# Kernel tuning notes

Measured on AMD Instinct MI355X. Metric: run time of the kernel, lower is better.

The kernel has to match this reference:

```python
import jax, jax.numpy as jnp
import numpy as np

H = 2048      # hidden_size
NH = 16       # num_attention_heads
HD = H // NH  # head_dim = 128
B, S = 2, 2048
ROPE_BASE = 10000.0


def setup_inputs() -> dict:
    key = jax.random.key(0)
    ks = jax.random.split(key, 9)
    init = 0.02
    inp = {
        "hidden_states": jax.random.normal(ks[0], (B, S, H), dtype=jnp.float32),
        # torch nn.Linear weights are [out_features, in_features]
        "wq": jax.random.normal(ks[1], (H, H), dtype=jnp.float32) * init,
        "bq": jnp.zeros((H,), dtype=jnp.float32),
        "wk": jax.random.normal(ks[2], (H, H), dtype=jnp.float32) * init,
        "bk": jnp.zeros((H,), dtype=jnp.float32),
        "wv": jax.random.normal(ks[3], (H, H), dtype=jnp.float32) * init,
        "bv": jnp.zeros((H,), dtype=jnp.float32),
        "wo": jax.random.normal(ks[4], (H, H), dtype=jnp.float32) * init,
        "bo": jnp.zeros((H,), dtype=jnp.float32),
    }
    return inp


def _rope_cos_sin(seq_len, dim, dtype):
    # standard RoPE tables: [seq_len, dim]
    inv_freq = 1.0 / (ROPE_BASE ** (jnp.arange(0, dim, 2, dtype=jnp.float32) / dim))
    freqs = jnp.arange(seq_len, dtype=jnp.float32)[:, None] * inv_freq[None, :]
    emb = jnp.concatenate([freqs, freqs], axis=-1)  # [S, dim]
    return jnp.cos(emb).astype(dtype), jnp.sin(emb).astype(dtype)


def _rotate_half(x):
    half = x.shape[-1] // 2
    return jnp.concatenate([-x[..., half:], x[..., :half]], axis=-1)


def reference(hidden_states, wq, bq, wk, bk, wv, bv, wo, bo):
    b, s, h = hidden_states.shape
    scale = HD ** -0.5

    def proj(x, w, bias):
        y = jnp.einsum("bsh,oh->bso", x, w) + bias
        # -> [b, nh, s, hd]
        return y.reshape(b, s, NH, HD).transpose(0, 2, 1, 3)

    q = proj(hidden_states, wq, bq)
    k = proj(hidden_states, wk, bk)
    v = proj(hidden_states, wv, bv)

    # rotary embeddings on q, k
    cos, sin = _rope_cos_sin(s, HD, q.dtype)  # [s, hd]
    q = q * cos + _rotate_half(q) * sin
    k = k * cos + _rotate_half(k) * sin

    # causal additive mask [s, s]
    mask = jnp.triu(jnp.full((s, s), -1e9, dtype=q.dtype), k=1)

    scores = jnp.einsum("bhqd,bhkd->bhqk", q, k) * scale + mask
    probs = jax.nn.softmax(scores, axis=-1)
    attn = jnp.einsum("bhqk,bhkd->bhqd", probs, v)
    attn = attn.transpose(0, 2, 1, 3).reshape(b, s, h)
    out = jnp.einsum("bsh,oh->bso", attn, wo) + bo
    return out
```

## Files before the change

### kernel.cpp

```cpp
#include <hip/hip_runtime.h>

typedef unsigned short u16;
typedef __attribute__((ext_vector_type(8))) __bf16 bf16x8;
typedef __attribute__((ext_vector_type(4))) float f32x4;
typedef __attribute__((ext_vector_type(4))) u16 u16x4;
typedef __attribute__((ext_vector_type(8))) u16 u16x8;

constexpr int S = 2048;
constexpr int H = 2048;
constexpr int NH = 16;
constexpr int HD = 128;
constexpr int M = 4096;
constexpr float SCALE = 0.08838834764831845f;

__device__ __forceinline__ u16 f2bf(float f) {
  union { float f; unsigned u; } v; v.f = f;
  unsigned r = v.u + 0x7fffu + ((v.u >> 16) & 1u);
  return (u16)(r >> 16);
}
__device__ __forceinline__ float bf2f(u16 u) {
  union { unsigned u; float f; } v; v.u = ((unsigned)u) << 16;
  return v.f;
}
__device__ __forceinline__ unsigned cvt_pk_bf16(float lo, float hi) {
  unsigned r;
  asm("v_cvt_pk_bf16_f32 %0, %1, %2" : "=v"(r) : "v"(lo), "v"(hi));
  return r;
}

__device__ __forceinline__ void gld16(const u16* g, u16* l) {
  __builtin_amdgcn_global_load_lds(
      (const __attribute__((address_space(1))) void*)g,
      (__attribute__((address_space(3))) void*)l, 16, 0, 0);
}

__global__ __launch_bounds__(256) void cast_kernel(const float* __restrict__ in,
                                                   u16* __restrict__ out, int n) {
  int i = (blockIdx.x * 256 + threadIdx.x) * 4;
  if (i >= n) return;
  float4 v = *(const float4*)(in + i);
  u16x4 o;
  o[0] = f2bf(v.x); o[1] = f2bf(v.y); o[2] = f2bf(v.z); o[3] = f2bf(v.w);
  *(u16x4*)(out + i) = o;
}

__global__ __launch_bounds__(256) void cast4_kernel(const float* __restrict__ i0,
                                                    const float* __restrict__ i1,
                                                    const float* __restrict__ i2,
                                                    const float* __restrict__ i3,
                                                    u16* o0, u16* o1, u16* o2, u16* o3) {
  const float* in; u16* out;
  switch (blockIdx.y) {
    case 0: in = i0; out = o0; break;
    case 1: in = i1; out = o1; break;
    case 2: in = i2; out = o2; break;
    default: in = i3; out = o3; break;
  }
  int i = (blockIdx.x * 256 + threadIdx.x) * 4;
  float4 v = *(const float4*)(in + i);
  u16x4 o;
  o[0] = f2bf(v.x); o[1] = f2bf(v.y); o[2] = f2bf(v.z); o[3] = f2bf(v.w);
  *(u16x4*)(out + i) = o;
}

__global__ __launch_bounds__(256) void rope_table_k(float* __restrict__ tab) {
  int i = blockIdx.x * 256 + threadIdx.x;
  if (i >= S * 64) return;
  int s = i >> 6, d = i & 63;
  float freq = expf(-(float)d * (9.210340371976184f / 64.f));
  float ang = (float)s * freq;
  tab[i * 2]     = cosf(ang);
  tab[i * 2 + 1] = sinf(ang);
}

__global__ __launch_bounds__(256) void rope_apply2_k(u16* __restrict__ Qb, u16* __restrict__ Kb,
                                                     const float* __restrict__ tab) {
  u16* X = blockIdx.y ? Kb : Qb;
  const float sc = blockIdx.y ? 1.f : SCALE;
  int i = blockIdx.x * 256 + threadIdx.x;
  int j0 = (i & 7) * 8;
  int h  = (i >> 3) & 15;
  int m  = i >> 7;
  int s  = m & (S - 1);
  u16* p = X + (size_t)m * H + h * HD;
  u16x8 lo = *(u16x8*)(p + j0);
  u16x8 hi = *(u16x8*)(p + 64 + j0);
  u16x8 nlo, nhi;
  const float* tb = tab + ((size_t)s * 64 + j0) * 2;
  #pragma unroll
  for (int j = 0; j < 8; ++j) {
    float c = tb[j * 2], sn = tb[j * 2 + 1];
    float xl = bf2f(lo[j]), xh = bf2f(hi[j]);
    nlo[j] = f2bf((xl * c - xh * sn) * sc);
    nhi[j] = f2bf((xh * c + xl * sn) * sc);
  }
  *(u16x8*)(p + j0) = nlo;
  *(u16x8*)(p + 64 + j0) = nhi;
}


__global__ __launch_bounds__(256) void gemm_qkv(const u16* __restrict__ A,
                                                const u16* __restrict__ Wq,
                                                const u16* __restrict__ Wk,
                                                const u16* __restrict__ Wv,
                                                const float* __restrict__ bq,
                                                const float* __restrict__ bk,
                                                const float* __restrict__ bv,
                                                u16* __restrict__ Qb,
                                                u16* __restrict__ Kb,
                                                u16* __restrict__ Vt) {
  __shared__ u16 As[128 * 32];
  __shared__ u16 Bs[128 * 32];
  const int z = blockIdx.z;
  const u16* Bw = (z == 0) ? Wq : (z == 1) ? Wk : Wv;
  const float* bias = (z == 0) ? bq : (z == 1) ? bk : bv;
  const int t = threadIdx.x;
  const int w = t >> 6, l = t & 63;
  const int wr = w >> 1, wc = w & 1;
  const int lr = l & 15, lg = l >> 4;
  const int brow = blockIdx.y * 128, bcol = blockIdx.x * 128;

  f32x4 acc[4][4] = {};

  const int srow = t >> 2;
  const int scol = (t & 3) * 8;
  const u16* ga = A  + (size_t)(brow + srow) * H + scol;
  const u16* gb = Bw + (size_t)(bcol + srow) * H + scol;
  u16* la = As + srow * 32 + scol;
  u16* lb = Bs + srow * 32 + scol;

  for (int kt = 0; kt < H; kt += 32) {
    gld16(ga + kt,          la);
    gld16(ga + kt + 64 * H, la + 64 * 32);
    gld16(gb + kt,          lb);
    gld16(gb + kt + 64 * H, lb + 64 * 32);
    __syncthreads();
    bf16x8 af[4], bf[4];
    #pragma unroll
    for (int m = 0; m < 4; ++m)
      af[m] = *(const bf16x8*)(As + (wr * 64 + m * 16 + lr) * 32 + lg * 8);
    #pragma unroll
    for (int n = 0; n < 4; ++n)
      bf[n] = *(const bf16x8*)(Bs + (wc * 64 + n * 16 + lr) * 32 + lg * 8);
    #pragma unroll
    for (int m = 0; m < 4; ++m)
      #pragma unroll
      for (int n = 0; n < 4; ++n)
        acc[m][n] = __builtin_amdgcn_mfma_f32_16x16x32_bf16(af[m], bf[n], acc[m][n], 0, 0, 0);
    __syncthreads();
  }

  #pragma unroll
  for (int m = 0; m < 4; ++m) {
    const int row0 = brow + wr * 64 + m * 16 + lg * 4;
    #pragma unroll
    for (int n = 0; n < 4; ++n) {
      const int col = bcol + wc * 64 + n * 16 + lr;
      const float bv2 = bias[col];
      if (z < 2) {
        u16* C = z ? Kb : Qb;
        #pragma unroll
        for (int r = 0; r < 4; ++r)
          C[(size_t)(row0 + r) * H + col] = f2bf(acc[m][n][r] + bv2);
      } else {
        const int hh = col >> 7, d = col & 127;
        const int b = row0 >> 11, s0 = row0 & (S - 1);
        u16x4 pk;
        #pragma unroll
        for (int r = 0; r < 4; ++r) pk[r] = f2bf(acc[m][n][r] + bv2);
        *(u16x4*)(Vt + ((size_t)((b * 16 + hh) * 128 + d)) * S + s0) = pk;
      }
    }
  }
}

__global__ __launch_bounds__(256) void gemm_out(const u16* __restrict__ A,
                                                const u16* __restrict__ Bw,
                                                const float* __restrict__ bias,
                                                float* __restrict__ Cout) {
  __shared__ u16 As[128 * 32];
  __shared__ u16 Bs[128 * 32];
  const int t = threadIdx.x;
  const int w = t >> 6, l = t & 63;
  const int wr = w >> 1, wc = w & 1;
  const int lr = l & 15, lg = l >> 4;
  const int brow = blockIdx.y * 128, bcol = blockIdx.x * 128;

  f32x4 acc[4][4] = {};

  const int srow = t >> 2;
  const int scol = (t & 3) * 8;
  const u16* ga = A  + (size_t)(brow + srow) * H + scol;
  const u16* gb = Bw + (size_t)(bcol + srow) * H + scol;
  u16* la = As + srow * 32 + scol;
  u16* lb = Bs + srow * 32 + scol;

  for (int kt = 0; kt < H; kt += 32) {
    gld16(ga + kt,          la);
    gld16(ga + kt + 64 * H, la + 64 * 32);
    gld16(gb + kt,          lb);
    gld16(gb + kt + 64 * H, lb + 64 * 32);
    __syncthreads();
    bf16x8 af[4], bf[4];
    #pragma unroll
    for (int m = 0; m < 4; ++m)
      af[m] = *(const bf16x8*)(As + (wr * 64 + m * 16 + lr) * 32 + lg * 8);
    #pragma unroll
    for (int n = 0; n < 4; ++n)
      bf[n] = *(const bf16x8*)(Bs + (wc * 64 + n * 16 + lr) * 32 + lg * 8);
    #pragma unroll
    for (int m = 0; m < 4; ++m)
      #pragma unroll
      for (int n = 0; n < 4; ++n)
        acc[m][n] = __builtin_amdgcn_mfma_f32_16x16x32_bf16(af[m], bf[n], acc[m][n], 0, 0, 0);
    __syncthreads();
  }

  #pragma unroll
  for (int m = 0; m < 4; ++m) {
    const int row0 = brow + wr * 64 + m * 16 + lg * 4;
    #pragma unroll
    for (int n = 0; n < 4; ++n) {
      const int col = bcol + wc * 64 + n * 16 + lr;
      const float bv2 = bias[col];
      #pragma unroll
      for (int r = 0; r < 4; ++r)
        Cout[(size_t)(row0 + r) * H + col] = acc[m][n][r] + bv2;
    }
  }
}

__global__ __launch_bounds__(256) void attn_fwd(const u16* __restrict__ Q,
                                                const u16* __restrict__ Kx,
                                                const u16* __restrict__ Vt,
                                                u16* __restrict__ O) {
  const int id = blockIdx.x;
  const int xcd = id & 7, slot = id >> 3;
  const int bh = (slot >> 4) * 8 + xcd;
  const int pid = slot & 15;
  const int b = bh >> 4, h = bh & 15;
  const int t = threadIdx.x, w = t >> 6, l = t & 63;
  const int lr = l & 15, lg = l >> 4;
  const int swz = lr & 7;

  __shared__ u16 Ks[2][64 * 128];
  __shared__ u16 Vs[2][128 * 64];
  __shared__ u16 P_lds[4][16 * 64];
  u16* pw = &P_lds[w][0];

  const u16* kbase = Kx + (size_t)(b * S) * H + h * HD;
  const u16* vbase = Vt + (size_t)bh * HD * S;

  auto stageK = [&](int bf, int k0) {
    #pragma unroll
    for (int it = 0; it < 4; ++it) {
      int c = it * 256 + t;
      int row = c >> 4, j = c & 15;
      gld16(kbase + (size_t)(k0 + row) * H + ((j ^ (row & 7)) * 8), &Ks[bf][0] + c * 8);
    }
  };
  auto stageV = [&](int bf, int k0) {
    #pragma unroll
    for (int it = 0; it < 4; ++it) {
      int c = it * 256 + t;
      int row = c >> 3, j = c & 7;
      gld16(vbase + (size_t)row * S + k0 + ((j ^ (row & 7)) * 8), &Vs[bf][0] + c * 8);
    }
  };

  int cur = 0;
  for (int qi = 0; qi < 2; ++qi) {
    const int qt = qi ? pid : (31 - pid);
    const int q0 = qt * 64 + w * 16;

    bf16x8 qa[4];
    const u16* qbase = Q + (size_t)(b * S + q0 + lr) * H + h * HD;
    #pragma unroll
    for (int ks = 0; ks < 4; ++ks)
      qa[ks] = *(const bf16x8*)(qbase + ks * 32 + lg * 8);

    f32x4 acc[8] = {};
    float mrun[4], lrun[4];
    #pragma unroll
    for (int r = 0; r < 4; ++r) { mrun[r] = -1e30f; lrun[r] = 0.f; }

    __syncthreads();
    stageK(cur, 0);
    stageV(cur, 0);
    __syncthreads();

    for (int kt = 0; kt <= qt; ++kt) {
      if (kt < qt) {
        stageK(cur ^ 1, (kt + 1) * 64);
        stageV(cur ^ 1, (kt + 1) * 64);
      }
      const u16* kl = &Ks[cur][0];
      const u16* vl = &Vs[cur][0];

      f32x4 sc[4] = {};
      __builtin_amdgcn_s_setprio(1);
      #pragma unroll
      for (int ks = 0; ks < 4; ++ks) {
        #pragma unroll
        for (int f = 0; f < 4; ++f) {
          bf16x8 kf = *(const bf16x8*)(kl + (f * 16 + lr) * 128 + (((ks * 4 + lg) ^ swz) * 8));
          sc[f] = __builtin_amdgcn_mfma_f32_16x16x32_bf16(qa[ks], kf, sc[f], 0, 0, 0);
        }
      }
      __builtin_amdgcn_s_setprio(0);
      const bool diag = (kt == qt);
      float p[4][4];
      #pragma unroll
      for (int f = 0; f < 4; ++f)
        #pragma unroll
        for (int r = 0; r < 4; ++r) {
          float v = sc[f][r];
          if (diag && (f * 16 + lr > w * 16 + lg * 4 + r)) v = -1e30f;
          p[f][r] = v;
        }
      float mx[4];
      #pragma unroll
      for (int r = 0; r < 4; ++r) {
        float m0 = fmaxf(fmaxf(p[0][r], p[1][r]), fmaxf(p[2][r], p[3][r]));
        m0 = fmaxf(m0, __shfl_xor(m0, 1));
        m0 = fmaxf(m0, __shfl_xor(m0, 2));
        m0 = fmaxf(m0, __shfl_xor(m0, 4));
        m0 = fmaxf(m0, __shfl_xor(m0, 8));
        mx[r] = m0;
      }
      bool grow = (mx[0] > mrun[0] + 8.f) || (mx[1] > mrun[1] + 8.f) ||
                  (mx[2] > mrun[2] + 8.f) || (mx[3] > mrun[3] + 8.f);
      if (__any(grow)) {
        float resc[4];
        #pragma unroll
        for (int r = 0; r < 4; ++r) {
          float mnew = fmaxf(mrun[r], mx[r]);
          resc[r] = __expf(mrun[r] - mnew);
          mrun[r] = mnew;
          lrun[r] *= resc[r];
        }
        #pragma unroll
        for (int fd = 0; fd < 8; ++fd) {
          f32x4 a = acc[fd];
          a[0] *= resc[0]; a[1] *= resc[1]; a[2] *= resc[2]; a[3] *= resc[3];
          acc[fd] = a;
        }
      }
      #pragma unroll
      for (int r = 0; r < 4; ++r) {
        float sum = 0.f;
        #pragma unroll
        for (int f = 0; f < 4; ++f) {
          float e = __expf(p[f][r] - mrun[r]);
          p[f][r] = e;
          sum += e;
        }
        sum += __shfl_xor(sum, 1);
        sum += __shfl_xor(sum, 2);
        sum += __shfl_xor(sum, 4);
        sum += __shfl_xor(sum, 8);
        lrun[r] += sum;
      }
      {
        const int r0 = lg * 4;
        #pragma unroll
        for (int f = 0; f < 4; ++f) {
          const int col = f * 16 + lr;
          unsigned w01 = cvt_pk_bf16(p[f][0], p[f][1]);
          unsigned w23 = cvt_pk_bf16(p[f][2], p[f][3]);
          pw[(r0 + 0) * 64 + (col ^ (((r0 + 0) & 7) << 3))] = (u16)(w01 & 0xffffu);
          pw[(r0 + 1) * 64 + (col ^ (((r0 + 1) & 7) << 3))] = (u16)(w01 >> 16);
          pw[(r0 + 2) * 64 + (col ^ (((r0 + 2) & 7) << 3))] = (u16)(w23 & 0xffffu);
          pw[(r0 + 3) * 64 + (col ^ (((r0 + 3) & 7) << 3))] = (u16)(w23 >> 16);
        }
      }
      __builtin_amdgcn_s_setprio(1);
      #pragma unroll
      for (int ks = 0; ks < 2; ++ks) {
        int col0 = ks * 32 + lg * 8;
        bf16x8 pa = *(const bf16x8*)(pw + lr * 64 + (col0 ^ (swz << 3)));
        #pragma unroll
        for (int fd = 0; fd < 8; ++fd) {
          bf16x8 vb = *(const bf16x8*)(vl + (fd * 16 + lr) * 64 + (((ks * 4 + lg) ^ swz) * 8));
          acc[fd] = __builtin_amdgcn_mfma_f32_16x16x32_bf16(pa, vb, acc[fd], 0, 0, 0);
        }
      }
      __builtin_amdgcn_s_setprio(0);
      __syncthreads();
      cur ^= 1;
    }

    u16* ob = O + (size_t)(b * S + q0 + lg * 4) * H + h * HD;
    #pragma unroll
    for (int r = 0; r < 4; ++r) {
      float inv = 1.f / lrun[r];
      #pragma unroll
      for (int fd = 0; fd < 8; ++fd)
        ob[(size_t)r * H + fd * 16 + lr] = f2bf(acc[fd][r] * inv);
    }
  }
}

extern "C" void kernel_launch(void* const* d_in, const int* in_sizes, int n_in,
                              void* d_out, int out_size, void* d_ws, size_t ws_size,
                              hipStream_t stream) {
  const float* x  = (const float*)d_in[0];
  const float* wq = (const float*)d_in[1];
  const float* bq = (const float*)d_in[2];
  const float* wk = (const float*)d_in[3];
  const float* bk = (const float*)d_in[4];
  const float* wv = (const float*)d_in[5];
  const float* bv = (const float*)d_in[6];
  const float* wo = (const float*)d_in[7];
  const float* bo = (const float*)d_in[8];

  char* ws = (char*)d_ws;
  u16*   xb  = (u16*)(ws);
  u16*   wqb = (u16*)(ws + (16ull << 20));
  u16*   wkb = (u16*)(ws + (24ull << 20));
  u16*   wvb = (u16*)(ws + (32ull << 20));
  u16*   wob = (u16*)(ws + (40ull << 20));
  u16*   Qb  = (u16*)(ws + (48ull << 20));
  u16*   Kb  = (u16*)(ws + (64ull << 20));
  u16*   Vt  = (u16*)(ws + (80ull << 20));
  u16*   Ob  = (u16*)(ws + (96ull << 20));
  float* tab = (float*)(ws + (112ull << 20));

  cast_kernel<<<M * H / 1024, 256, 0, stream>>>(x, xb, M * H);
  cast4_kernel<<<dim3(H * H / 1024, 4), 256, 0, stream>>>(wq, wk, wv, wo, wqb, wkb, wvb, wob);
  rope_table_k<<<(S * 64 + 255) / 256, 256, 0, stream>>>(tab);

  gemm_qkv<<<dim3(H / 128, M / 128, 3), 256, 0, stream>>>(xb, wqb, wkb, wvb, bq, bk, bv, Qb, Kb, Vt);

  rope_apply2_k<<<dim3(M * NH * 8 / 256, 2), 256, 0, stream>>>(Qb, Kb, tab);

  attn_fwd<<<dim3(512), 256, 0, stream>>>(Qb, Kb, Vt, Ob);

  gemm_out<<<dim3(H / 128, M / 128), 256, 0, stream>>>(Ob, wob, bo, (float*)d_out);
}
```

Baseline: 314.9 us.

## Replace QKV and output GEMMs with 256x256 8-wave pipelined GEMM

Both projection GEMMs are replaced by a shared 256x256-tile kernel that uses 512 threads, a BK=64 double-buffered LDS pipeline, XOR-swizzled LDS layout and explicit waitcnt/barrier scheduling. Blocks are remapped across XCDs. The larger tiles raise arithmetic intensity, and the interleaved global-to-LDS staging is meant to hide memory latency behind MFMA work. The costs are heavy register pressure (32 accumulators per lane) and 128 KB of LDS per block. The output GEMM also launches only 128 blocks, which may underfill the GPU.

Result: slower. 328.3 us (+4.3%).

```diff
diff --git a/kernel.cpp b/kernel.cpp
--- a/kernel.cpp
+++ b/kernel.cpp
@@ -27,12 +27,19 @@
   asm("v_cvt_pk_bf16_f32 %0, %1, %2" : "=v"(r) : "v"(lo), "v"(hi));
   return r;
 }
+__device__ __forceinline__ f32x4 MFMA16(bf16x8 a, bf16x8 b, f32x4 c) {
+  return __builtin_amdgcn_mfma_f32_16x16x32_bf16(a, b, c, 0, 0, 0);
+}
 
 __device__ __forceinline__ void gld16(const u16* g, u16* l) {
   __builtin_amdgcn_global_load_lds(
       (const __attribute__((address_space(1))) void*)g,
       (__attribute__((address_space(3))) void*)l, 16, 0, 0);
 }
+
+#define SBAR  { __builtin_amdgcn_sched_barrier(0); __builtin_amdgcn_s_barrier(); __builtin_amdgcn_sched_barrier(0); }
+#define LGKM0 { asm volatile("s_waitcnt lgkmcnt(0)" ::: "memory"); __builtin_amdgcn_sched_barrier(0); }
+#define VM(N) { asm volatile("s_waitcnt vmcnt(" #N ")" ::: "memory"); }
 
 __global__ __launch_bounds__(256) void cast_kernel(const float* __restrict__ in,
                                                    u16* __restrict__ out, int n) {
@@ -98,136 +105,173 @@
   *(u16x8*)(p + 64 + j0) = nhi;
 }
 
-
-__global__ __launch_bounds__(256) void gemm_qkv(const u16* __restrict__ A,
-                                                const u16* __restrict__ Wq,
-                                                const u16* __restrict__ Wk,
-                                                const u16* __restrict__ Wv,
-                                                const float* __restrict__ bq,
-                                                const float* __restrict__ bk,
-                                                const float* __restrict__ bv,
-                                                u16* __restrict__ Qb,
-                                                u16* __restrict__ Kb,
-                                                u16* __restrict__ Vt) {
-  __shared__ u16 As[128 * 32];
-  __shared__ u16 Bs[128 * 32];
-  const int z = blockIdx.z;
-  const u16* Bw = (z == 0) ? Wq : (z == 1) ? Wk : Wv;
-  const float* bias = (z == 0) ? bq : (z == 1) ? bk : bv;
+__device__ __forceinline__ void gemm8_body(const u16* __restrict__ srcA,
+                                           const u16* __restrict__ srcB,
+                                           const float* __restrict__ bias,
+                                           void* __restrict__ Cout,
+                                           int emode, int brow, int bcol,
+                                           u16* AsL, u16* BsL) {
   const int t = threadIdx.x;
   const int w = t >> 6, l = t & 63;
-  const int wr = w >> 1, wc = w & 1;
+  const int wr = w >> 2, wc = w & 3;
   const int lr = l & 15, lg = l >> 4;
-  const int brow = blockIdx.y * 128, bcol = blockIdx.x * 128;
-
-  f32x4 acc[4][4] = {};
-
-  const int srow = t >> 2;
-  const int scol = (t & 3) * 8;
-  const u16* ga = A  + (size_t)(brow + srow) * H + scol;
-  const u16* gb = Bw + (size_t)(bcol + srow) * H + scol;
-  u16* la = As + srow * 32 + scol;
-  u16* lb = Bs + srow * 32 + scol;
-
-  for (int kt = 0; kt < H; kt += 32) {
-    gld16(ga + kt,          la);
-    gld16(ga + kt + 64 * H, la + 64 * 32);
-    gld16(gb + kt,          lb);
-    gld16(gb + kt + 64 * H, lb + 64 * 32);
-    __syncthreads();
-    bf16x8 af[4], bf[4];
-    #pragma unroll
-    for (int m = 0; m < 4; ++m)
-      af[m] = *(const bf16x8*)(As + (wr * 64 + m * 16 + lr) * 32 + lg * 8);
-    #pragma unroll
-    for (int n = 0; n < 4; ++n)
-      bf[n] = *(const bf16x8*)(Bs + (wc * 64 + n * 16 + lr) * 32 + lg * 8);
-    #pragma unroll
-    for (int m = 0; m < 4; ++m)
-      #pragma unroll
-      for (int n = 0; n < 4; ++n)
-        acc[m][n] = __builtin_amdgcn_mfma_f32_16x16x32_bf16(af[m], bf[n], acc[m][n], 0, 0, 0);
-    __syncthreads();
+  const int swz = lr & 7;
+
+  f32x4 acc[8][4] = {};
+  bf16x8 af[4][2], bA[2][2], bB[2][2];
+
+  const int c0r = t >> 3,        c0j = t & 7;
+  const int c1r = 64 + (t >> 3), c1j = t & 7;
+
+  #define STAGE(SRC, DSTB, BUF, HALF, TILE) do {                                   \
+    u16* _d = (DSTB) + (BUF) * (256 * 64) + (HALF) * (128 * 64);                   \
+    const u16* _s = (SRC) + ((size_t)((HALF) * 128)) * H + (TILE) * 64;            \
+    gld16(_s + (size_t)c0r * H + ((c0j ^ (c0r & 7)) * 8), _d + t * 8);             \
+    gld16(_s + (size_t)c1r * H + ((c1j ^ (c1r & 7)) * 8), _d + (512 + t) * 8);     \
+  } while (0)
+
+  #define LDA4(BUF, MB) do {                                                       \
+    const u16* _b = AsL + (BUF) * (256 * 64) + (wr * 128 + lr) * 64;               \
+    _Pragma("unroll") for (int i = 0; i < 4; ++i) {                                \
+      af[i][0] = *(const bf16x8*)(_b + ((MB) + i) * (16 * 64) + ((lg ^ swz) * 8)); \
+      af[i][1] = *(const bf16x8*)(_b + ((MB) + i) * (16 * 64) + (((4 + lg) ^ swz) * 8)); \
+    } } while (0)
+
+  #define LDB2(BUF, BF, NB) do {                                                   \
+    const u16* _b = BsL + (BUF) * (256 * 64) + (wc * 64 + lr) * 64;                \
+    _Pragma("unroll") for (int i = 0; i < 2; ++i) {                                \
+      BF[i][0] = *(const bf16x8*)(_b + ((NB) + i) * (16 * 64) + ((lg ^ swz) * 8)); \
+      BF[i][1] = *(const bf16x8*)(_b + ((NB) + i) * (16 * 64) + (((4 + lg) ^ swz) * 8)); \
+    } } while (0)
+
+  #define MM16(MB, BF, NB) do {                                                    \
+    __builtin_amdgcn_s_setprio(1);                                                 \
+    _Pragma("unroll") for (int i = 0; i < 4; ++i)                                  \
+      _Pragma("unroll") for (int n = 0; n < 2; ++n) {                              \
+        acc[(MB) + i][(NB) + n] = MFMA16(af[i][0], BF[n][0], acc[(MB) + i][(NB) + n]); \
+        acc[(MB) + i][(NB) + n] = MFMA16(af[i][1], BF[n][1], acc[(MB) + i][(NB) + n]); \
+      }                                                                            \
+    __builtin_amdgcn_s_setprio(0);                                                 \
+  } while (0)
+
+  STAGE(srcB, BsL, 0, 0, 0); STAGE(srcB, BsL, 0, 1, 0);
+  STAGE(srcA, AsL, 0, 0, 0); STAGE(srcA, AsL, 0, 1, 0);
+  STAGE(srcB, BsL, 1, 0, 1);
+  VM(2);
+  SBAR;
+
+  for (int J = 0; J < 16; ++J) {
+    const int u = 2 * J;
+    const bool more = (J < 15);
+    LDA4(0, 0); LDB2(0, bA, 0);
+    STAGE(srcB, BsL, 1, 1, u + 1);
+    SBAR; LGKM0;
+    MM16(0, bA, 0);
+    SBAR;
+    LDA4(0, 4);
+    STAGE(srcA, AsL, 1, 0, u + 1);
+    SBAR; LGKM0;
+    MM16(4, bA, 0);
+    SBAR;
+    LDB2(0, bB, 2);
+    STAGE(srcA, AsL, 1, 1, u + 1);
+    SBAR; LGKM0;
+    MM16(4, bB, 2);
+    SBAR;
+    LDA4(0, 0);
+    if (more) STAGE(srcB, BsL, 0, 0, u + 2);
+    SBAR; LGKM0;
+    MM16(0, bB, 2);
+    if (more) { VM(2); } else { VM(0); }
+    SBAR;
+    LDA4(1, 0); LDB2(1, bA, 0);
+    if (more) STAGE(srcB, BsL, 0, 1, u + 2);
+    SBAR; LGKM0;
+    MM16(0, bA, 0);
+    SBAR;
+    LDA4(1, 4);
+    if (more) STAGE(srcA, AsL, 0, 0, u + 2);
+    SBAR; LGKM0;
+    MM16(4, bA, 0);
+    SBAR;
+    LDB2(1, bB, 2);
+    if (more) STAGE(srcA, AsL, 0, 1, u + 2);
+    SBAR; LGKM0;
+    MM16(4, bB, 2);
+    SBAR;
+    LDA4(1, 0);
+    if (more) STAGE(srcB, BsL, 1, 0, u + 3);
+    SBAR; LGKM0;
+    MM16(0, bB, 2);
+    if (more) VM(2);
+    SBAR;
   }
 
   #pragma unroll
-  for (int m = 0; m < 4; ++m) {
-    const int row0 = brow + wr * 64 + m * 16 + lg * 4;
+  for (int m = 0; m < 8; ++m) {
+    const int row0 = brow + wr * 128 + m * 16 + lg * 4;
     #pragma unroll
     for (int n = 0; n < 4; ++n) {
       const int col = bcol + wc * 64 + n * 16 + lr;
-      const float bv2 = bias[col];
-      if (z < 2) {
-        u16* C = z ? Kb : Qb;
+      const float bv = bias[col];
+      if (emode == 0) {
+        float* C = (float*)Cout;
         #pragma unroll
         for (int r = 0; r < 4; ++r)
-          C[(size_t)(row0 + r) * H + col] = f2bf(acc[m][n][r] + bv2);
+          C[(size_t)(row0 + r) * H + col] = acc[m][n][r] + bv;
+      } else if (emode == 1) {
+        u16* C = (u16*)Cout;
+        #pragma unroll
+        for (int r = 0; r < 4; ++r)
+          C[(size_t)(row0 + r) * H + col] = f2bf(acc[m][n][r] + bv);
       } else {
         const int hh = col >> 7, d = col & 127;
         const int b = row0 >> 11, s0 = row0 & (S - 1);
         u16x4 pk;
         #pragma unroll
-        for (int r = 0; r < 4; ++r) pk[r] = f2bf(acc[m][n][r] + bv2);
-        *(u16x4*)(Vt + ((size_t)((b * 16 + hh) * 128 + d)) * S + s0) = pk;
+        for (int r = 0; r < 4; ++r) pk[r] = f2bf(acc[m][n][r] + bv);
+        *(u16x4*)((u16*)Cout + ((size_t)((b * 16 + hh) * 128 + d)) * S + s0) = pk;
       }
     }
   }
-}
-
-__global__ __launch_bounds__(256) void gemm_out(const u16* __restrict__ A,
-                                                const u16* __restrict__ Bw,
-                                                const float* __restrict__ bias,
-                                                float* __restrict__ Cout) {
-  __shared__ u16 As[128 * 32];
-  __shared__ u16 Bs[128 * 32];
-  const int t = threadIdx.x;
-  const int w = t >> 6, l = t & 63;
-  const int wr = w >> 1, wc = w & 1;
-  const int lr = l & 15, lg = l >> 4;
-  const int brow = blockIdx.y * 128, bcol = blockIdx.x * 128;
-
-  f32x4 acc[4][4] = {};
-
-  const int srow = t >> 2;
-  const int scol = (t & 3) * 8;
-  const u16* ga = A  + (size_t)(brow + srow) * H + scol;
-  const u16* gb = Bw + (size_t)(bcol + srow) * H + scol;
-  u16* la = As + srow * 32 + scol;
-  u16* lb = Bs + srow * 32 + scol;
-
-  for (int kt = 0; kt < H; kt += 32) {
-    gld16(ga + kt,          la);
-    gld16(ga + kt + 64 * H, la + 64 * 32);
-    gld16(gb + kt,          lb);
-    gld16(gb + kt + 64 * H, lb + 64 * 32);
-    __syncthreads();
-    bf16x8 af[4], bf[4];
-    #pragma unroll
-    for (int m = 0; m < 4; ++m)
-      af[m] = *(const bf16x8*)(As + (wr * 64 + m * 16 + lr) * 32 + lg * 8);
-    #pragma unroll
-    for (int n = 0; n < 4; ++n)
-      bf[n] = *(const bf16x8*)(Bs + (wc * 64 + n * 16 + lr) * 32 + lg * 8);
-    #pragma unroll
-    for (int m = 0; m < 4; ++m)
-      #pragma unroll
-      for (int n = 0; n < 4; ++n)
-        acc[m][n] = __builtin_amdgcn_mfma_f32_16x16x32_bf16(af[m], bf[n], acc[m][n], 0, 0, 0);
-    __syncthreads();
-  }
-
-  #pragma unroll
-  for (int m = 0; m < 4; ++m) {
-    const int row0 = brow + wr * 64 + m * 16 + lg * 4;
-    #pragma unroll
-    for (int n = 0; n < 4; ++n) {
-      const int col = bcol + wc * 64 + n * 16 + lr;
-      const float bv2 = bias[col];
-      #pragma unroll
-      for (int r = 0; r < 4; ++r)
-        Cout[(size_t)(row0 + r) * H + col] = acc[m][n][r] + bv2;
-    }
-  }
+  #undef STAGE
+  #undef LDA4
+  #undef LDB2
+  #undef MM16
+}
+
+__global__ __launch_bounds__(512, 2) void gemm8_qkv(const u16* __restrict__ xb,
+                                                    const u16* __restrict__ wqb,
+                                                    const u16* __restrict__ wkb,
+                                                    const u16* __restrict__ wvb,
+                                                    const float* __restrict__ bq,
+                                                    const float* __restrict__ bk,
+                                                    const float* __restrict__ bv,
+                                                    u16* Qb, u16* Kb, u16* Vt) {
+  __shared__ u16 AsL[2 * 256 * 64];
+  __shared__ u16 BsL[2 * 256 * 64];
+  const int id = blockIdx.x;
+  const int lin = (id & 7) * 48 + (id >> 3);
+  const int bz = lin >> 7, rem = lin & 127;
+  const int bx = rem & 7, by = rem >> 3;
+  const u16* Bw = (bz == 0) ? wqb : (bz == 1) ? wkb : wvb;
+  const float* bias = (bz == 0) ? bq : (bz == 1) ? bk : bv;
+  void* out = (bz == 0) ? (void*)Qb : (bz == 1) ? (void*)Kb : (void*)Vt;
+  gemm8_body(xb + (size_t)(by * 256) * H, Bw + (size_t)(bx * 256) * H,
+             bias, out, (bz == 2) ? 2 : 1, by * 256, bx * 256, AsL, BsL);
+}
+
+__global__ __launch_bounds__(512, 2) void gemm8_out(const u16* __restrict__ A,
+                                                    const u16* __restrict__ W,
+                                                    const float* __restrict__ bias,
+                                                    float* __restrict__ C) {
+  __shared__ u16 AsL[2 * 256 * 64];
+  __shared__ u16 BsL[2 * 256 * 64];
+  const int id = blockIdx.x;
+  const int lin = (id & 7) * 16 + (id >> 3);
+  const int bx = lin & 7, by = lin >> 3;
+  gemm8_body(A + (size_t)(by * 256) * H, W + (size_t)(bx * 256) * H,
+             bias, (void*)C, 0, by * 256, bx * 256, AsL, BsL);
 }
 
 __global__ __launch_bounds__(256) void attn_fwd(const u16* __restrict__ Q,
@@ -430,11 +474,11 @@
   cast4_kernel<<<dim3(H * H / 1024, 4), 256, 0, stream>>>(wq, wk, wv, wo, wqb, wkb, wvb, wob);
   rope_table_k<<<(S * 64 + 255) / 256, 256, 0, stream>>>(tab);
 
-  gemm_qkv<<<dim3(H / 128, M / 128, 3), 256, 0, stream>>>(xb, wqb, wkb, wvb, bq, bk, bv, Qb, Kb, Vt);
+  gemm8_qkv<<<384, 512, 0, stream>>>(xb, wqb, wkb, wvb, bq, bk, bv, Qb, Kb, Vt);
 
   rope_apply2_k<<<dim3(M * NH * 8 / 256, 2), 256, 0, stream>>>(Qb, Kb, tab);
 
-  attn_fwd<<<dim3(512), 256, 0, stream>>>(Qb, Kb, Vt, Ob);
-
-  gemm_out<<<dim3(H / 128, M / 128), 256, 0, stream>>>(Ob, wob, bo, (float*)d_out);
-}
+  attn_fwd<<<512, 256, 0, stream>>>(Qb, Kb, Vt, Ob);
+
+  gemm8_out<<<128, 512, 0, stream>>>(Ob, wob, bo, (float*)d_out);
+}
```

## Rewrite projection GEMMs as 8-wave double-buffered pipelined kernels with fused QKV weight

Applied to the files above, without the earlier changes.

Replaces the simple 128x128 single-buffered QKV and output GEMMs with a shared templated body using 512 threads, 256-row tiles, K=64 double-buffered LDS with XOR swizzle, explicit waitcnt/barrier scheduling and MFMA priority. The Q, K and V weights are cast into one concatenated matrix and the biases concatenated, so a single GEMM with 192-wide column tiles covers all three projections. Block IDs are remapped per XCD for L2 locality. The aim is better MFMA utilisation and load/compute overlap, at the cost of fragile hand-tuned vmcnt gating and higher register and LDS pressure.

Result: faster. 275.5 us (-12.5%).

```diff
diff --git a/kernel.cpp b/kernel.cpp
--- a/kernel.cpp
+++ b/kernel.cpp
@@ -27,12 +27,18 @@
   asm("v_cvt_pk_bf16_f32 %0, %1, %2" : "=v"(r) : "v"(lo), "v"(hi));
   return r;
 }
+__device__ __forceinline__ f32x4 MFMA16(bf16x8 a, bf16x8 b, f32x4 c) {
+  return __builtin_amdgcn_mfma_f32_16x16x32_bf16(a, b, c, 0, 0, 0);
+}
 
 __device__ __forceinline__ void gld16(const u16* g, u16* l) {
   __builtin_amdgcn_global_load_lds(
       (const __attribute__((address_space(1))) void*)g,
       (__attribute__((address_space(3))) void*)l, 16, 0, 0);
 }
+
+#define SBAR  { __builtin_amdgcn_sched_barrier(0); __builtin_amdgcn_s_barrier(); __builtin_amdgcn_sched_barrier(0); }
+#define LGKM0 { asm volatile("s_waitcnt lgkmcnt(0)" ::: "memory"); __builtin_amdgcn_sched_barrier(0); }
 
 __global__ __launch_bounds__(256) void cast_kernel(const float* __restrict__ in,
                                                    u16* __restrict__ out, int n) {
@@ -61,6 +67,15 @@
   u16x4 o;
   o[0] = f2bf(v.x); o[1] = f2bf(v.y); o[2] = f2bf(v.z); o[3] = f2bf(v.w);
   *(u16x4*)(out + i) = o;
+}
+
+__global__ __launch_bounds__(256) void concat_bias_k(const float* __restrict__ bq,
+                                                     const float* __restrict__ bk,
+                                                     const float* __restrict__ bv,
+                                                     float* __restrict__ bqkv) {
+  int i = blockIdx.x * 256 + threadIdx.x;
+  const float* src = (i < 2048) ? bq : (i < 4096) ? bk : bv;
+  bqkv[i] = src[i & 2047];
 }
 
 __global__ __launch_bounds__(256) void rope_table_k(float* __restrict__ tab) {
@@ -98,136 +113,156 @@
   *(u16x8*)(p + 64 + j0) = nhi;
 }
 
-
-__global__ __launch_bounds__(256) void gemm_qkv(const u16* __restrict__ A,
-                                                const u16* __restrict__ Wq,
-                                                const u16* __restrict__ Wk,
-                                                const u16* __restrict__ Wv,
-                                                const float* __restrict__ bq,
-                                                const float* __restrict__ bk,
-                                                const float* __restrict__ bv,
-                                                u16* __restrict__ Qb,
-                                                u16* __restrict__ Kb,
-                                                u16* __restrict__ Vt) {
-  __shared__ u16 As[128 * 32];
-  __shared__ u16 Bs[128 * 32];
-  const int z = blockIdx.z;
-  const u16* Bw = (z == 0) ? Wq : (z == 1) ? Wk : Wv;
-  const float* bias = (z == 0) ? bq : (z == 1) ? bk : bv;
+template<int NW, int EMODE>
+__device__ __forceinline__ void gemm_body(const u16* __restrict__ A,
+                                          const u16* __restrict__ Bw,
+                                          const float* __restrict__ bias,
+                                          void* __restrict__ out0, void* __restrict__ out1,
+                                          void* __restrict__ out2,
+                                          int brow, int bcol,
+                                          u16* AsL, u16* BsL) {
   const int t = threadIdx.x;
   const int w = t >> 6, l = t & 63;
-  const int wr = w >> 1, wc = w & 1;
+  const int wr = w >> 2, wc = w & 3;
   const int lr = l & 15, lg = l >> 4;
-  const int brow = blockIdx.y * 128, bcol = blockIdx.x * 128;
-
-  f32x4 acc[4][4] = {};
-
-  const int srow = t >> 2;
-  const int scol = (t & 3) * 8;
-  const u16* ga = A  + (size_t)(brow + srow) * H + scol;
-  const u16* gb = Bw + (size_t)(bcol + srow) * H + scol;
-  u16* la = As + srow * 32 + scol;
-  u16* lb = Bs + srow * 32 + scol;
-
-  for (int kt = 0; kt < H; kt += 32) {
-    gld16(ga + kt,          la);
-    gld16(ga + kt + 64 * H, la + 64 * 32);
-    gld16(gb + kt,          lb);
-    gld16(gb + kt + 64 * H, lb + 64 * 32);
-    __syncthreads();
-    bf16x8 af[4], bf[4];
-    #pragma unroll
-    for (int m = 0; m < 4; ++m)
-      af[m] = *(const bf16x8*)(As + (wr * 64 + m * 16 + lr) * 32 + lg * 8);
-    #pragma unroll
-    for (int n = 0; n < 4; ++n)
-      bf[n] = *(const bf16x8*)(Bs + (wc * 64 + n * 16 + lr) * 32 + lg * 8);
-    #pragma unroll
-    for (int m = 0; m < 4; ++m)
-      #pragma unroll
-      for (int n = 0; n < 4; ++n)
-        acc[m][n] = __builtin_amdgcn_mfma_f32_16x16x32_bf16(af[m], bf[n], acc[m][n], 0, 0, 0);
-    __syncthreads();
+  const int swz = lr & 7;
+
+  f32x4 acc[8][NW] = {};
+  bf16x8 af[4], b0[NW], b1[NW];
+
+  const int sr = t >> 3, sj = t & 7;
+
+  auto STAGE_A = [&](int BUF, int HALF, int TILE) {
+    u16* d = AsL + BUF * (256 * 64) + HALF * (128 * 64);
+    const u16* sp = A + (size_t)(brow + HALF * 128) * H + TILE * 64;
+    gld16(sp + (size_t)sr * H        + ((sj ^ (sr & 7)) * 8), d + t * 8);
+    gld16(sp + (size_t)(64 + sr) * H + ((sj ^ (sr & 7)) * 8), d + (512 + t) * 8);
+  };
+  auto STAGE_B = [&](int BUF, int TILE) {
+    u16* d = BsL + BUF * (NW * 64 * 64);
+    const u16* sp = Bw + (size_t)bcol * H + TILE * 64;
+    #pragma unroll
+    for (int i = 0; i < NW; ++i)
+      gld16(sp + (size_t)(i * 64 + sr) * H + ((sj ^ (sr & 7)) * 8),
+            d + (i * 512 + t) * 8);
+  };
+  auto LDA = [&](int BUF, int KH, int MB) {
+    const u16* base = AsL + BUF * (256 * 64) + (wr * 128 + MB * 16 + lr) * 64;
+    #pragma unroll
+    for (int i = 0; i < 4; ++i)
+      af[i] = *(const bf16x8*)(base + i * (16 * 64) + (((KH * 4 + lg) ^ swz) * 8));
+  };
+  auto LDB = [&](int BUF, int KH, bf16x8* bb) {
+    const u16* base = BsL + BUF * (NW * 64 * 64) + (wc * (NW * 16) + lr) * 64;
+    #pragma unroll
+    for (int n = 0; n < NW; ++n)
+      bb[n] = *(const bf16x8*)(base + n * (16 * 64) + (((KH * 4 + lg) ^ swz) * 8));
+  };
+  auto MM = [&](int MB, bf16x8* bb) {
+    __builtin_amdgcn_s_setprio(1);
+    #pragma unroll
+    for (int i = 0; i < 4; ++i)
+      #pragma unroll
+      for (int n = 0; n < NW; ++n)
+        acc[MB + i][n] = MFMA16(af[i], bb[n], acc[MB + i][n]);
+    __builtin_amdgcn_s_setprio(0);
+  };
+  auto GATE = [&]() {
+    if constexpr (NW == 3) { asm volatile("s_waitcnt vmcnt(3)" ::: "memory"); }
+    else                   { asm volatile("s_waitcnt vmcnt(2)" ::: "memory"); }
+  };
+
+  STAGE_A(0, 0, 0); STAGE_A(0, 1, 0);
+  STAGE_B(0, 0);
+  STAGE_B(1, 1);
+  GATE();
+  SBAR;
+
+  for (int J = 0; J < 16; ++J) {
+    const int u = 2 * J;
+    const bool more = (J < 15);
+    LDA(0, 0, 0); LDB(0, 0, b0);
+    STAGE_A(1, 0, u + 1);
+    SBAR; LGKM0; MM(0, b0); SBAR;
+    LDA(0, 0, 4);
+    STAGE_A(1, 1, u + 1);
+    SBAR; LGKM0; MM(4, b0); SBAR;
+    LDA(0, 1, 0); LDB(0, 1, b1);
+    SBAR; LGKM0; MM(0, b1); SBAR;
+    LDA(0, 1, 4);
+    if (more) STAGE_B(0, u + 2);
+    SBAR; LGKM0; MM(4, b1);
+    if (more) { GATE(); } else { asm volatile("s_waitcnt vmcnt(0)" ::: "memory"); }
+    SBAR;
+    LDA(1, 0, 0); LDB(1, 0, b0);
+    if (more) STAGE_A(0, 0, u + 2);
+    SBAR; LGKM0; MM(0, b0); SBAR;
+    LDA(1, 0, 4);
+    if (more) STAGE_A(0, 1, u + 2);
+    SBAR; LGKM0; MM(4, b0); SBAR;
+    LDA(1, 1, 0); LDB(1, 1, b1);
+    SBAR; LGKM0; MM(0, b1); SBAR;
+    LDA(1, 1, 4);
+    if (more) STAGE_B(1, u + 3);
+    SBAR; LGKM0; MM(4, b1);
+    if (more) { GATE(); SBAR; }
   }
 
   #pragma unroll
-  for (int m = 0; m < 4; ++m) {
-    const int row0 = brow + wr * 64 + m * 16 + lg * 4;
-    #pragma unroll
-    for (int n = 0; n < 4; ++n) {
-      const int col = bcol + wc * 64 + n * 16 + lr;
-      const float bv2 = bias[col];
-      if (z < 2) {
-        u16* C = z ? Kb : Qb;
+  for (int m = 0; m < 8; ++m) {
+    const int row0 = brow + wr * 128 + m * 16 + lg * 4;
+    #pragma unroll
+    for (int n = 0; n < NW; ++n) {
+      const int gcol0 = bcol + wc * (NW * 16) + n * 16;
+      const float bv = bias[gcol0 + lr];
+      if constexpr (EMODE == 0) {
+        float* C = (float*)out0;
         #pragma unroll
         for (int r = 0; r < 4; ++r)
-          C[(size_t)(row0 + r) * H + col] = f2bf(acc[m][n][r] + bv2);
+          C[(size_t)(row0 + r) * H + gcol0 + lr] = acc[m][n][r] + bv;
       } else {
-        const int hh = col >> 7, d = col & 127;
-        const int b = row0 >> 11, s0 = row0 & (S - 1);
-        u16x4 pk;
-        #pragma unroll
-        for (int r = 0; r < 4; ++r) pk[r] = f2bf(acc[m][n][r] + bv2);
-        *(u16x4*)(Vt + ((size_t)((b * 16 + hh) * 128 + d)) * S + s0) = pk;
+        const int sel = gcol0 >> 11;
+        const int col = (gcol0 & 2047) + lr;
+        if (sel < 2) {
+          u16* C = sel ? (u16*)out1 : (u16*)out0;
+          #pragma unroll
+          for (int r = 0; r < 4; ++r)
+            C[(size_t)(row0 + r) * H + col] = f2bf(acc[m][n][r] + bv);
+        } else {
+          const int hh = col >> 7, d = col & 127;
+          const int b = row0 >> 11, s0 = row0 & (S - 1);
+          u16x4 pk;
+          #pragma unroll
+          for (int r = 0; r < 4; ++r) pk[r] = f2bf(acc[m][n][r] + bv);
+          *(u16x4*)((u16*)out2 + ((size_t)((b * 16 + hh) * 128 + d)) * S + s0) = pk;
+        }
       }
     }
   }
 }
 
-__global__ __launch_bounds__(256) void gemm_out(const u16* __restrict__ A,
-                                                const u16* __restrict__ Bw,
-                                                const float* __restrict__ bias,
-                                                float* __restrict__ Cout) {
-  __shared__ u16 As[128 * 32];
-  __shared__ u16 Bs[128 * 32];
-  const int t = threadIdx.x;
-  const int w = t >> 6, l = t & 63;
-  const int wr = w >> 1, wc = w & 1;
-  const int lr = l & 15, lg = l >> 4;
-  const int brow = blockIdx.y * 128, bcol = blockIdx.x * 128;
-
-  f32x4 acc[4][4] = {};
-
-  const int srow = t >> 2;
-  const int scol = (t & 3) * 8;
-  const u16* ga = A  + (size_t)(brow + srow) * H + scol;
-  const u16* gb = Bw + (size_t)(bcol + srow) * H + scol;
-  u16* la = As + srow * 32 + scol;
-  u16* lb = Bs + srow * 32 + scol;
-
-  for (int kt = 0; kt < H; kt += 32) {
-    gld16(ga + kt,          la);
-    gld16(ga + kt + 64 * H, la + 64 * 32);
-    gld16(gb + kt,          lb);
-    gld16(gb + kt + 64 * H, lb + 64 * 32);
-    __syncthreads();
-    bf16x8 af[4], bf[4];
-    #pragma unroll
-    for (int m = 0; m < 4; ++m)
-      af[m] = *(const bf16x8*)(As + (wr * 64 + m * 16 + lr) * 32 + lg * 8);
-    #pragma unroll
-    for (int n = 0; n < 4; ++n)
-      bf[n] = *(const bf16x8*)(Bs + (wc * 64 + n * 16 + lr) * 32 + lg * 8);
-    #pragma unroll
-    for (int m = 0; m < 4; ++m)
-      #pragma unroll
-      for (int n = 0; n < 4; ++n)
-        acc[m][n] = __builtin_amdgcn_mfma_f32_16x16x32_bf16(af[m], bf[n], acc[m][n], 0, 0, 0);
-    __syncthreads();
-  }
-
-  #pragma unroll
-  for (int m = 0; m < 4; ++m) {
-    const int row0 = brow + wr * 64 + m * 16 + lg * 4;
-    #pragma unroll
-    for (int n = 0; n < 4; ++n) {
-      const int col = bcol + wc * 64 + n * 16 + lr;
-      const float bv2 = bias[col];
-      #pragma unroll
-      for (int r = 0; r < 4; ++r)
-        Cout[(size_t)(row0 + r) * H + col] = acc[m][n][r] + bv2;
-    }
-  }
+__global__ __launch_bounds__(512, 2) void gemm_qkv8(const u16* __restrict__ xb,
+                                                    const u16* __restrict__ wqkv,
+                                                    const float* __restrict__ bqkv,
+                                                    u16* Qb, u16* Kb, u16* Vt) {
+  __shared__ u16 AsL[2 * 256 * 64];
+  __shared__ u16 BsL[2 * 192 * 64];
+  const int id = blockIdx.x;
+  const int xcd = id & 7, sid = id >> 3;
+  const int bx = xcd * 4 + (sid & 3), by = sid >> 2;
+  gemm_body<3, 3>(xb, wqkv, bqkv, Qb, Kb, Vt, by * 256, bx * 192, AsL, BsL);
+}
+
+__global__ __launch_bounds__(512, 2) void gemm_o8(const u16* __restrict__ A,
+                                                  const u16* __restrict__ W,
+                                                  const float* __restrict__ bias,
+                                                  float* __restrict__ C) {
+  __shared__ u16 AsL[2 * 256 * 64];
+  __shared__ u16 BsL[2 * 128 * 64];
+  const int id = blockIdx.x;
+  const int xcd = id & 7, sid = id >> 3;
+  const int bx = xcd * 2 + (sid & 1), by = sid >> 1;
+  gemm_body<2, 0>(A, W, bias, C, nullptr, nullptr, by * 256, bx * 128, AsL, BsL);
 }
 
 __global__ __launch_bounds__(256) void attn_fwd(const u16* __restrict__ Q,
@@ -415,26 +450,27 @@
   const float* bo = (const float*)d_in[8];
 
   char* ws = (char*)d_ws;
-  u16*   xb  = (u16*)(ws);
-  u16*   wqb = (u16*)(ws + (16ull << 20));
-  u16*   wkb = (u16*)(ws + (24ull << 20));
-  u16*   wvb = (u16*)(ws + (32ull << 20));
-  u16*   wob = (u16*)(ws + (40ull << 20));
-  u16*   Qb  = (u16*)(ws + (48ull << 20));
-  u16*   Kb  = (u16*)(ws + (64ull << 20));
-  u16*   Vt  = (u16*)(ws + (80ull << 20));
-  u16*   Ob  = (u16*)(ws + (96ull << 20));
-  float* tab = (float*)(ws + (112ull << 20));
+  u16*   xb    = (u16*)(ws);
+  u16*   wqkvb = (u16*)(ws + (16ull << 20));
+  u16*   wob   = (u16*)(ws + (40ull << 20));
+  u16*   Qb    = (u16*)(ws + (48ull << 20));
+  u16*   Kb    = (u16*)(ws + (64ull << 20));
+  u16*   Vt    = (u16*)(ws + (80ull << 20));
+  u16*   Ob    = (u16*)(ws + (96ull << 20));
+  float* tab   = (float*)(ws + (112ull << 20));
+  float* bqkv  = (float*)(ws + (113ull << 20));
 
   cast_kernel<<<M * H / 1024, 256, 0, stream>>>(x, xb, M * H);
-  cast4_kernel<<<dim3(H * H / 1024, 4), 256, 0, stream>>>(wq, wk, wv, wo, wqb, wkb, wvb, wob);
+  cast4_kernel<<<dim3(H * H / 1024, 4), 256, 0, stream>>>(
+      wq, wk, wv, wo, wqkvb, wqkvb + (size_t)H * H, wqkvb + 2ull * H * H, wob);
   rope_table_k<<<(S * 64 + 255) / 256, 256, 0, stream>>>(tab);
-
-  gemm_qkv<<<dim3(H / 128, M / 128, 3), 256, 0, stream>>>(xb, wqb, wkb, wvb, bq, bk, bv, Qb, Kb, Vt);
+  concat_bias_k<<<24, 256, 0, stream>>>(bq, bk, bv, bqkv);
+
+  gemm_qkv8<<<512, 512, 0, stream>>>(xb, wqkvb, bqkv, Qb, Kb, Vt);
 
   rope_apply2_k<<<dim3(M * NH * 8 / 256, 2), 256, 0, stream>>>(Qb, Kb, tab);
 
-  attn_fwd<<<dim3(512), 256, 0, stream>>>(Qb, Kb, Vt, Ob);
-
-  gemm_out<<<dim3(H / 128, M / 128), 256, 0, stream>>>(Ob, wob, bo, (float*)d_out);
-}
+  attn_fwd<<<512, 256, 0, stream>>>(Qb, Kb, Vt, Ob);
+
+  gemm_o8<<<256, 512, 0, stream>>>(Ob, wob, bo, (float*)d_out);
+}
```
